# Kernel optimization log

Hardware: AMD Instinct MI355X
Metric: run time of the kernel (lower is better)

The kernel has to match this reference:

```python
import jax, jax.numpy as jnp
import numpy as np

HEADS = 16
PHI = (1.0 + np.sqrt(5.0)) / 2.0


def setup_inputs() -> dict:
    key = jax.random.key(0)
    k1, k2, k3, k4 = jax.random.split(key, 4)
    B, L, D = 2, 2048, 1024
    x = jax.random.normal(k1, (B, L, D), dtype=jnp.float32)
    # nn.Linear(dim, 3*dim, bias=False): store as [D, 3D] for x @ W
    w_qkv = jax.random.normal(k2, (D, 3 * D), dtype=jnp.float32) * (D ** -0.5)
    w_proj = jax.random.normal(k3, (D, D), dtype=jnp.float32) * (D ** -0.5)
    b_proj = jax.random.normal(k4, (D,), dtype=jnp.float32) * 0.01
    return {"x": x, "w_qkv": w_qkv, "w_proj": w_proj, "b_proj": b_proj}


def phi_bias(L):
    # pos[i] = (i * phi) mod 1 ; bias = log(exp(-|pos_i - pos_j|) + 1e-8)
    pos = (jnp.arange(L, dtype=jnp.float32) * PHI) % 1.0
    dist = jnp.abs(pos[:, None] - pos[None, :])  # [L, L]
    return jnp.log(jnp.exp(-dist) + 1e-8)


def reference(x, w_qkv, w_proj, b_proj):
    B, L, D = x.shape
    H = HEADS
    Dh = D // H
    scale = Dh ** -0.5
    qkv = (x @ w_qkv).reshape(B, L, 3, H, Dh)
    q = jnp.transpose(qkv[:, :, 0], (0, 2, 1, 3))  # [B, H, L, Dh]
    k = jnp.transpose(qkv[:, :, 1], (0, 2, 1, 3))
    v = jnp.transpose(qkv[:, :, 2], (0, 2, 1, 3))
    attn = jnp.einsum("bhid,bhjd->bhij", q, k) * scale  # [B, H, L, L]
    attn = attn + phi_bias(L)[None, None]  # additive phi-distance bias
    attn = jax.nn.softmax(attn, axis=-1)
    out = jnp.einsum("bhij,bhjd->bhid", attn, v)  # [B, H, L, Dh]
    out = jnp.transpose(out, (0, 2, 1, 3)).reshape(B, L, D)
    return out @ w_proj + b_proj
```

## Files before the change

### kernel.cpp

```cpp
#include <hip/hip_runtime.h>
#include <math.h>


typedef _Float16 f16;
typedef _Float16 f16x4 __attribute__((ext_vector_type(4)));
typedef _Float16 f16x8 __attribute__((ext_vector_type(8)));
typedef float f32x4 __attribute__((ext_vector_type(4)));

#define MFMA32(a, b, c) __builtin_amdgcn_mfma_f32_16x16x32_f16(a, b, c, 0, 0, 0)

static constexpr int Bsz = 2, Lseq = 2048, Dm = 1024, H = 16, Dh = 64;
static constexpr int Mtot = Bsz * Lseq;
static constexpr int NQKV = 3 * Dm;
static constexpr float PHI_F = 1.61803398874989484820f;
static constexpr float LOG2E = 1.44269504088896f;
static constexpr float QS = 0.125f * LOG2E;
static constexpr float CSTEP = 0.55417527999932633f;

__device__ __forceinline__ void load16_to_lds(const f16* g, f16* l) {
  __builtin_amdgcn_global_load_lds(
      (const __attribute__((address_space(1))) unsigned int*)g,
      (__attribute__((address_space(3))) unsigned int*)l, 16, 0, 0);
}

__device__ __forceinline__ void barrier_fenced() {
  __builtin_amdgcn_sched_barrier(0);
  __builtin_amdgcn_s_barrier();
  __builtin_amdgcn_sched_barrier(0);
}

__global__ __launch_bounds__(256) void prep_fused(
    const float* __restrict__ x, f16* __restrict__ xb,
    const float* __restrict__ wqkv, f16* __restrict__ wqkvT,
    const float* __restrict__ wproj, f16* __restrict__ wpT) {
  __shared__ float tile[32][33];
  int blk = blockIdx.x;
  if (blk < 4096) {
    int i = (blk * 256 + threadIdx.x) * 4;
    float4 v = *reinterpret_cast<const float4*>(x + i);
    f16 t[4] = {(f16)v.x, (f16)v.y, (f16)v.z, (f16)v.w};
    *reinterpret_cast<uint2*>(xb + i) = *reinterpret_cast<uint2*>(t);
    return;
  }
  const float* in;
  f16* out;
  int N, bx, by;
  if (blk < 7168) {
    int local = blk - 4096;
    bx = local % 96; by = local / 96; N = NQKV;
    in = wqkv; out = wqkvT;
  } else {
    int local = blk - 7168;
    bx = local & 31; by = local >> 5; N = Dm;
    in = wproj; out = wpT;
  }
  int n0 = bx * 32, k0 = by * 32;
  int tx = threadIdx.x & 31, ty = threadIdx.x >> 5;
#pragma unroll
  for (int r = 0; r < 32; r += 8)
    tile[ty + r][tx] = in[(size_t)(k0 + ty + r) * N + n0 + tx];
  __syncthreads();
#pragma unroll
  for (int r = 0; r < 32; r += 8)
    out[(size_t)(n0 + ty + r) * Dm + k0 + tx] = (f16)tile[tx][ty + r];
}

__global__ __launch_bounds__(512, 2) void gemm_qkv(
    const f16* __restrict__ A, const f16* __restrict__ Bt,
    f16* __restrict__ qb, f16* __restrict__ kb, f16* __restrict__ vb) {
  __shared__ f16 As[2 * 256 * 64];
  __shared__ f16 Bs[2 * 256 * 64];

  int tid = threadIdx.x;
  int wave = tid >> 6, lane = tid & 63;
  int quad = lane >> 4, l16 = lane & 15;
  int warp_m = wave >> 2, warp_n = wave & 3;
  int wm = warp_m * 128, wn = warp_n * 64;

  int lid = blockIdx.x;
  int xcd = lid & 7, t = lid >> 3;
  int mg = xcd >> 1, ng = xcd & 1;
  int m0 = (mg * 4 + t / 6) * 256;
  int n0 = (ng * 6 + t % 6) * 256;

  const int gu = (lane & 7) ^ (lane >> 3);
  const f16* gAb = A + (size_t)(m0 + wave * 8 + (lane >> 3)) * Dm + gu * 8;
  const f16* gBb = Bt + (size_t)(n0 + wave * 8 + (lane >> 3)) * Dm + gu * 8;

  auto stageA = [&](int buf, int h, int kn) __attribute__((always_inline)) {
#pragma unroll
    for (int i = 0; i < 2; i++)
      load16_to_lds(gAb + (size_t)(h * 128 + i * 64) * Dm + kn,
                    As + buf * 16384 + (h * 128 + i * 64 + wave * 8) * 64);
  };
  auto stageB = [&](int buf, int h, int kn) __attribute__((always_inline)) {
#pragma unroll
    for (int i = 0; i < 2; i++)
      load16_to_lds(gBb + (size_t)(h * 128 + i * 64) * Dm + kn,
                    Bs + buf * 16384 + (h * 128 + i * 64 + wave * 8) * 64);
  };

  f32x4 acc[8][4] = {};

  auto do_tile = [&](int buf, int t_) __attribute__((always_inline)) {
    const f16* Ab = As + buf * 16384 + (wm + l16) * 64;
    const f16* Bb = Bs + buf * 16384 + (wn + l16) * 64;
    int nbuf = buf ^ 1;
    int kA = ((t_ + 1) & 15) * 64;
    int kB = ((t_ + 2) & 15) * 64;

    f16x8 a[4][2], b0[2][2], b1[2][2];

#pragma unroll
    for (int m = 0; m < 4; m++)
#pragma unroll
      for (int s = 0; s < 2; s++)
        a[m][s] = *reinterpret_cast<const f16x8*>(
            Ab + m * 16 * 64 + (((s * 4 + quad) ^ (l16 & 7)) * 8));
#pragma unroll
    for (int n = 0; n < 2; n++)
#pragma unroll
      for (int s = 0; s < 2; s++)
        b0[n][s] = *reinterpret_cast<const f16x8*>(
            Bb + n * 16 * 64 + (((s * 4 + quad) ^ (l16 & 7)) * 8));
    stageA(nbuf, 0, kA);
    barrier_fenced();
    asm volatile("s_waitcnt lgkmcnt(0)" ::: "memory");
    __builtin_amdgcn_sched_barrier(0);
    __builtin_amdgcn_s_setprio(1);
#pragma unroll
    for (int m = 0; m < 4; m++)
#pragma unroll
      for (int n = 0; n < 2; n++) {
        acc[m][n] = MFMA32(a[m][0], b0[n][0], acc[m][n]);
        acc[m][n] = MFMA32(a[m][1], b0[n][1], acc[m][n]);
      }
    __builtin_amdgcn_s_setprio(0);
    barrier_fenced();

#pragma unroll
    for (int n = 0; n < 2; n++)
#pragma unroll
      for (int s = 0; s < 2; s++)
        b1[n][s] = *reinterpret_cast<const f16x8*>(
            Bb + (2 + n) * 16 * 64 + (((s * 4 + quad) ^ (l16 & 7)) * 8));
    stageA(nbuf, 1, kA);
    barrier_fenced();
    asm volatile("s_waitcnt lgkmcnt(0)" ::: "memory");
    __builtin_amdgcn_sched_barrier(0);
    __builtin_amdgcn_s_setprio(1);
#pragma unroll
    for (int m = 0; m < 4; m++)
#pragma unroll
      for (int n = 0; n < 2; n++) {
        acc[m][2 + n] = MFMA32(a[m][0], b1[n][0], acc[m][2 + n]);
        acc[m][2 + n] = MFMA32(a[m][1], b1[n][1], acc[m][2 + n]);
      }
    __builtin_amdgcn_s_setprio(0);
    barrier_fenced();

#pragma unroll
    for (int m = 0; m < 4; m++)
#pragma unroll
      for (int s = 0; s < 2; s++)
        a[m][s] = *reinterpret_cast<const f16x8*>(
            Ab + (4 + m) * 16 * 64 + (((s * 4 + quad) ^ (l16 & 7)) * 8));
    stageB(buf, 0, kB);
    barrier_fenced();
    asm volatile("s_waitcnt lgkmcnt(0)" ::: "memory");
    __builtin_amdgcn_sched_barrier(0);
    __builtin_amdgcn_s_setprio(1);
#pragma unroll
    for (int m = 0; m < 4; m++)
#pragma unroll
      for (int n = 0; n < 2; n++) {
        acc[4 + m][n] = MFMA32(a[m][0], b0[n][0], acc[4 + m][n]);
        acc[4 + m][n] = MFMA32(a[m][1], b0[n][1], acc[4 + m][n]);
      }
    __builtin_amdgcn_s_setprio(0);
    barrier_fenced();

    stageB(buf, 1, kB);
    asm volatile("s_waitcnt vmcnt(4)" ::: "memory");
    barrier_fenced();
    __builtin_amdgcn_s_setprio(1);
#pragma unroll
    for (int m = 0; m < 4; m++)
#pragma unroll
      for (int n = 0; n < 2; n++) {
        acc[4 + m][2 + n] = MFMA32(a[m][0], b1[n][0], acc[4 + m][2 + n]);
        acc[4 + m][2 + n] = MFMA32(a[m][1], b1[n][1], acc[4 + m][2 + n]);
      }
    __builtin_amdgcn_s_setprio(0);
    barrier_fenced();
  };

  stageA(0, 0, 0);
  stageA(0, 1, 0);
  stageB(0, 0, 0);
  stageB(0, 1, 0);
  stageB(1, 0, 64);
  stageB(1, 1, 64);
  asm volatile("s_waitcnt vmcnt(4)" ::: "memory");
  barrier_fenced();

#pragma unroll 1
  for (int tt = 0; tt < 16; tt += 2) {
    do_tile(0, tt);
    do_tile(1, tt + 1);
  }
  asm volatile("s_waitcnt vmcnt(0)" ::: "memory");

#pragma unroll
  for (int i = 0; i < 8; i++) {
#pragma unroll
    for (int j = 0; j < 4; j++) {
      int n = n0 + wn + j * 16 + l16;
      int ty = n >> 10;
      int df = n & 1023;
      int h = df >> 6, dh = df & 63;
      int mb = m0 + wm + i * 16 + quad * 4;
      int b = mb >> 11, l = mb & 2047;
      int bhh = b * H + h;
      if (ty == 2) {
        int jj = l & 63;
        int jh = jj >> 5, rem = jj & 31;
        int qd = (rem & 15) >> 2;
        int e0 = (rem >= 16) ? 4 : 0;
        f16x4 tmp;
#pragma unroll
        for (int r = 0; r < 4; r++) tmp[r] = (f16)acc[i][j][r];
        *reinterpret_cast<uint2*>(
            vb + (size_t)bhh * (Dh * Lseq) + (l >> 6) * 4096 + dh * 64 +
            (jh * 4 + qd) * 8 + e0) = *reinterpret_cast<uint2*>(&tmp);
      } else {
        size_t idx = (((size_t)bhh) * Lseq + l) * Dh + dh;
        if (ty == 0) {
#pragma unroll
          for (int r = 0; r < 4; r++)
            qb[idx + (size_t)r * Dh] = (f16)(acc[i][j][r] * QS);
        } else {
#pragma unroll
          for (int r = 0; r < 4; r++)
            kb[idx + (size_t)r * Dh] = (f16)acc[i][j][r];
        }
      }
    }
  }
}

__global__ __launch_bounds__(256) void gemm_proj(
    const f16* __restrict__ A, const f16* __restrict__ Bt,
    float* __restrict__ out, const float* __restrict__ bias) {
  constexpr int BM = 64, MI = 2, AI = 2;
  __shared__ f16 As[BM * 64];
  __shared__ f16 Bs[128 * 64];

  int tid = threadIdx.x;
  int wave = tid >> 6, lane = tid & 63;
  int quad = lane >> 4, l16 = lane & 15;
  int wm = (wave >> 1) * (MI * 16), wn = (wave & 1) * 64;

  int lid = blockIdx.x;
  int xcd = lid & 7, t = lid >> 3;
  int m0 = (xcd * 8 + (t >> 3)) * 64;
  int n0 = (t & 7) * 128;

  const int gu = (lane & 7) ^ (lane >> 3);
  const f16* gA[AI];
  f16* lA[AI];
#pragma unroll
  for (int i = 0; i < AI; i++) {
    int it = wave * AI + i;
    gA[i] = A + (size_t)(m0 + it * 8 + (lane >> 3)) * Dm + gu * 8;
    lA[i] = As + it * 512;
  }
  const f16* gB[4];
  f16* lB[4];
#pragma unroll
  for (int i = 0; i < 4; i++) {
    int it = wave * 4 + i;
    gB[i] = Bt + (size_t)(n0 + it * 8 + (lane >> 3)) * Dm + gu * 8;
    lB[i] = Bs + it * 512;
  }

  f32x4 acc[MI][4] = {};

  for (int k0 = 0; k0 < Dm; k0 += 64) {
#pragma unroll
    for (int i = 0; i < AI; i++) load16_to_lds(gA[i] + k0, lA[i]);
#pragma unroll
    for (int i = 0; i < 4; i++) load16_to_lds(gB[i] + k0, lB[i]);
    __syncthreads();
#pragma unroll
    for (int s = 0; s < 2; s++) {
      f16x8 a[MI], b[4];
#pragma unroll
      for (int i = 0; i < MI; i++) {
        int row = wm + i * 16 + l16;
        a[i] = *reinterpret_cast<const f16x8*>(
            As + row * 64 + (((s * 4 + quad) ^ (l16 & 7)) * 8));
      }
#pragma unroll
      for (int j = 0; j < 4; j++) {
        int row = wn + j * 16 + l16;
        b[j] = *reinterpret_cast<const f16x8*>(
            Bs + row * 64 + (((s * 4 + quad) ^ (l16 & 7)) * 8));
      }
#pragma unroll
      for (int i = 0; i < MI; i++)
#pragma unroll
        for (int j = 0; j < 4; j++)
          acc[i][j] = MFMA32(a[i], b[j], acc[i][j]);
    }
    __syncthreads();
  }

#pragma unroll
  for (int i = 0; i < MI; i++)
#pragma unroll
    for (int j = 0; j < 4; j++) {
      int n = n0 + wn + j * 16 + l16;
#pragma unroll
      for (int r = 0; r < 4; r++) {
        int m = m0 + wm + i * 16 + quad * 4 + r;
        out[(size_t)m * Dm + n] = acc[i][j][r] + bias[n];
      }
    }
}

__global__ __launch_bounds__(512, 4) void attn_kernel(
    const f16* __restrict__ qb,
    const f16* __restrict__ kb,
    const f16* __restrict__ vb,
    f16* __restrict__ ctx) {
  __shared__ __align__(16) unsigned char smem[33280];
  f16* Ks = (f16*)smem;
  f16* Vs = (f16*)(smem + 8192);

  int id = blockIdx.x;
  int bh = (id & 7) * 4 + ((id >> 3) >> 4);
  int q0 = ((id >> 3) & 15) * 128;

  int tid = threadIdx.x, wave = tid >> 6, lane = tid & 63;
  int quad = lane >> 4, l16 = lane & 15;
  int jhalf = wave >> 2, qq = wave & 3;

  f16x8 qfrag[2][2];
  float pq[2];
#pragma unroll
  for (int set = 0; set < 2; set++) {
    int q = q0 + qq * 32 + set * 16 + l16;
    const f16* Qrow = qb + ((size_t)bh * Lseq + q) * Dh;
    qfrag[set][0] = *reinterpret_cast<const f16x8*>(Qrow + quad * 8);
    qfrag[set][1] = *reinterpret_cast<const f16x8*>(Qrow + 32 + quad * 8);
    pq[set] = fmodf((float)q * PHI_F, 1.0f);
  }

  float pk[2][4];
#pragma unroll
  for (int jb = 0; jb < 2; jb++)
#pragma unroll
    for (int r = 0; r < 4; r++) {
      int j = jhalf * 32 + jb * 16 + quad * 4 + r;
      pk[jb][r] = fmodf((float)j * PHI_F, 1.0f);
    }

  const f16* Kbh = kb + (size_t)bh * Lseq * Dh;
  const f16* Vbh = vb + (size_t)bh * Dh * Lseq;
  const int gu = (lane & 7) ^ (lane >> 3);
  int g8 = wave * 8 + (lane >> 3);
  const f16* gK = Kbh + (size_t)g8 * Dh + gu * 8;
  const f16* gV = Vbh + (size_t)g8 * 64 + gu * 8;
  f16* lK = Ks + wave * 512;
  f16* lV = Vs + wave * 512;

  const f16 one = (f16)1.0f;
  const f16x8 ones8 = {one, one, one, one, one, one, one, one};

  f32x4 acc_o[2][4] = {};
  f32x4 acc_l[2] = {};

  for (int j0 = 0; j0 < Lseq; j0 += 64) {
    __syncthreads();
    load16_to_lds(gK + (size_t)j0 * Dh, lK);
    load16_to_lds(gV + (size_t)j0 * 64, lV);
    __syncthreads();

    f32x4 accs[2][2] = {};
#pragma unroll
    for (int s = 0; s < 2; s++)
#pragma unroll
      for (int jb = 0; jb < 2; jb++) {
        f16x8 kf = *reinterpret_cast<const f16x8*>(
            Ks + (jhalf * 32 + jb * 16 + l16) * 64 + (((s * 4 + quad) ^ (l16 & 7)) * 8));
        accs[0][jb] = MFMA32(kf, qfrag[0][s], accs[0][jb]);
        accs[1][jb] = MFMA32(kf, qfrag[1][s], accs[1][jb]);
      }

    f16x8 pf8[2];
#pragma unroll
    for (int set = 0; set < 2; set++) {
#pragma unroll
      for (int jb = 0; jb < 2; jb++) {
        float p[4];
#pragma unroll
        for (int r = 0; r < 4; r++) {
          float d = pq[set] - pk[jb][r];
          float arg = fmaf(-LOG2E, fabsf(d), accs[set][jb][r]);
          p[r] = __builtin_amdgcn_exp2f(arg);
        }
        auto lo = __builtin_amdgcn_cvt_pkrtz(p[0], p[1]);
        auto hi = __builtin_amdgcn_cvt_pkrtz(p[2], p[3]);
        pf8[set][jb * 4 + 0] = lo[0];
        pf8[set][jb * 4 + 1] = lo[1];
        pf8[set][jb * 4 + 2] = hi[0];
        pf8[set][jb * 4 + 3] = hi[1];
      }
      acc_l[set] = MFMA32(ones8, pf8[set], acc_l[set]);
    }
#pragma unroll
    for (int jb = 0; jb < 2; jb++)
#pragma unroll
      for (int r = 0; r < 4; r++)
        pk[jb][r] = __builtin_amdgcn_fractf(pk[jb][r] + CSTEP);

#pragma unroll
    for (int dblk = 0; dblk < 4; dblk++) {
      int row = dblk * 16 + l16;
      f16x8 va = *reinterpret_cast<const f16x8*>(
          Vs + row * 64 + (((jhalf * 4 + quad) ^ (l16 & 7)) * 8));
      acc_o[0][dblk] = MFMA32(va, pf8[0], acc_o[0][dblk]);
      acc_o[1][dblk] = MFMA32(va, pf8[1], acc_o[1][dblk]);
    }
  }

  __syncthreads();
  float* Oex = (float*)smem;
  float* Lex = (float*)(smem + 32768);
  if (jhalf == 1) {
#pragma unroll
    for (int set = 0; set < 2; set++) {
#pragma unroll
      for (int dblk = 0; dblk < 4; dblk++)
#pragma unroll
        for (int r = 0; r < 4; r++)
          Oex[(((qq * 2 + set) * 4 + dblk) * 16 + quad * 4 + r) * 16 + l16] =
              acc_o[set][dblk][r];
      if (quad == 0) Lex[(qq * 2 + set) * 16 + l16] = acc_l[set][0];
    }
  }
  __syncthreads();
  if (jhalf == 0) {
    int b = bh >> 4, h = bh & 15;
#pragma unroll
    for (int set = 0; set < 2; set++) {
      float ltot = acc_l[set][0] + Lex[(qq * 2 + set) * 16 + l16];
      float inv = 1.0f / ltot;
      int q = q0 + qq * 32 + set * 16 + l16;
      f16* crow = ctx + (size_t)(b * Lseq + q) * Dm + h * 64;
#pragma unroll
      for (int dblk = 0; dblk < 4; dblk++) {
        f16x4 o;
#pragma unroll
        for (int r = 0; r < 4; r++) {
          float full = acc_o[set][dblk][r] +
              Oex[(((qq * 2 + set) * 4 + dblk) * 16 + quad * 4 + r) * 16 + l16];
          o[r] = (f16)(full * inv);
        }
        *reinterpret_cast<uint2*>(crow + dblk * 16 + quad * 4) =
            *reinterpret_cast<uint2*>(&o);
      }
    }
  }
}

extern "C" void kernel_launch(void* const* d_in, const int* in_sizes, int n_in,
                              void* d_out, int out_size, void* d_ws, size_t ws_size,
                              hipStream_t stream) {
  const float* x      = (const float*)d_in[0];
  const float* w_qkv  = (const float*)d_in[1];
  const float* w_proj = (const float*)d_in[2];
  const float* b_proj = (const float*)d_in[3];
  float* out = (float*)d_out;

  f16* xb    = (f16*)d_ws;
  f16* wqkvT = xb + (size_t)Mtot * Dm;
  f16* wpT   = wqkvT + (size_t)NQKV * Dm;
  f16* qb    = wpT + (size_t)Dm * Dm;
  f16* kb    = qb + (size_t)Bsz * H * Lseq * Dh;
  f16* vb    = kb + (size_t)Bsz * H * Lseq * Dh;
  f16* ctx   = vb + (size_t)Bsz * H * Lseq * Dh;

  prep_fused<<<8192, 256, 0, stream>>>(x, xb, w_qkv, wqkvT, w_proj, wpT);

  gemm_qkv<<<192, 512, 0, stream>>>(xb, wqkvT, qb, kb, vb);

  attn_kernel<<<512, 512, 0, stream>>>(qb, kb, vb, ctx);

  gemm_proj<<<512, 256, 0, stream>>>(ctx, wpT, out, b_proj);
}
```

Baseline: 179.9 us.

## Retile QKV GEMM to 256x192 blocks so 256 blocks fill all CUs

Shrinks the QKV projection GEMM block tile from 256x256 to 256x192, so the grid grows from 192 to 256 blocks and maps onto all 256 compute units. The B staging, the MFMA loops, the accumulator shape, the vmcnt waits and the XCD-aware block swizzle are all reworked to match. This removes idle CUs in a single-wave launch, at the cost of lower arithmetic intensity per block and launch bounds relaxed to one block per CU.

```diff
diff --git a/kernel.cpp b/kernel.cpp
--- a/kernel.cpp
+++ b/kernel.cpp
@@ -65,23 +65,23 @@
     out[(size_t)(n0 + ty + r) * Dm + k0 + tx] = (f16)tile[tx][ty + r];
 }
 
-__global__ __launch_bounds__(512, 2) void gemm_qkv(
+__global__ __launch_bounds__(512, 1) void gemm_qkv(
     const f16* __restrict__ A, const f16* __restrict__ Bt,
     f16* __restrict__ qb, f16* __restrict__ kb, f16* __restrict__ vb) {
   __shared__ f16 As[2 * 256 * 64];
-  __shared__ f16 Bs[2 * 256 * 64];
+  __shared__ f16 Bs[2 * 192 * 64];
 
   int tid = threadIdx.x;
   int wave = tid >> 6, lane = tid & 63;
   int quad = lane >> 4, l16 = lane & 15;
   int warp_m = wave >> 2, warp_n = wave & 3;
-  int wm = warp_m * 128, wn = warp_n * 64;
+  int wm = warp_m * 128, wn = warp_n * 48;
 
   int lid = blockIdx.x;
   int xcd = lid & 7, t = lid >> 3;
-  int mg = xcd >> 1, ng = xcd & 1;
-  int m0 = (mg * 4 + t / 6) * 256;
-  int n0 = (ng * 6 + t % 6) * 256;
+  int mg = xcd & 3, ng = xcd >> 2;
+  int m0 = (mg * 4 + (t >> 3)) * 256;
+  int n0 = (ng * 8 + (t & 7)) * 192;
 
   const int gu = (lane & 7) ^ (lane >> 3);
   const f16* gAb = A + (size_t)(m0 + wave * 8 + (lane >> 3)) * Dm + gu * 8;
@@ -93,23 +93,28 @@
       load16_to_lds(gAb + (size_t)(h * 128 + i * 64) * Dm + kn,
                     As + buf * 16384 + (h * 128 + i * 64 + wave * 8) * 64);
   };
-  auto stageB = [&](int buf, int h, int kn) __attribute__((always_inline)) {
-#pragma unroll
-    for (int i = 0; i < 2; i++)
-      load16_to_lds(gBb + (size_t)(h * 128 + i * 64) * Dm + kn,
-                    Bs + buf * 16384 + (h * 128 + i * 64 + wave * 8) * 64);
+  auto stageB = [&](int buf, int part, int kn) __attribute__((always_inline)) {
+    if (part == 0) {
+#pragma unroll
+      for (int i = 0; i < 2; i++)
+        load16_to_lds(gBb + (size_t)(i * 64) * Dm + kn,
+                      Bs + buf * 12288 + (i * 64 + wave * 8) * 64);
+    } else {
+      load16_to_lds(gBb + (size_t)128 * Dm + kn,
+                    Bs + buf * 12288 + (128 + wave * 8) * 64);
+    }
   };
 
-  f32x4 acc[8][4] = {};
+  f32x4 acc[8][3] = {};
 
   auto do_tile = [&](int buf, int t_) __attribute__((always_inline)) {
     const f16* Ab = As + buf * 16384 + (wm + l16) * 64;
-    const f16* Bb = Bs + buf * 16384 + (wn + l16) * 64;
+    const f16* Bb = Bs + buf * 12288 + (wn + l16) * 64;
     int nbuf = buf ^ 1;
     int kA = ((t_ + 1) & 15) * 64;
     int kB = ((t_ + 2) & 15) * 64;
 
-    f16x8 a[4][2], b0[2][2], b1[2][2];
+    f16x8 a[4][2], b0[2][2], b1[2];
 
 #pragma unroll
     for (int m = 0; m < 4; m++)
@@ -139,23 +144,19 @@
     barrier_fenced();
 
 #pragma unroll
-    for (int n = 0; n < 2; n++)
-#pragma unroll
-      for (int s = 0; s < 2; s++)
-        b1[n][s] = *reinterpret_cast<const f16x8*>(
-            Bb + (2 + n) * 16 * 64 + (((s * 4 + quad) ^ (l16 & 7)) * 8));
+    for (int s = 0; s < 2; s++)
+      b1[s] = *reinterpret_cast<const f16x8*>(
+          Bb + 2 * 16 * 64 + (((s * 4 + quad) ^ (l16 & 7)) * 8));
     stageA(nbuf, 1, kA);
     barrier_fenced();
     asm volatile("s_waitcnt lgkmcnt(0)" ::: "memory");
     __builtin_amdgcn_sched_barrier(0);
     __builtin_amdgcn_s_setprio(1);
 #pragma unroll
-    for (int m = 0; m < 4; m++)
-#pragma unroll
-      for (int n = 0; n < 2; n++) {
-        acc[m][2 + n] = MFMA32(a[m][0], b1[n][0], acc[m][2 + n]);
-        acc[m][2 + n] = MFMA32(a[m][1], b1[n][1], acc[m][2 + n]);
-      }
+    for (int m = 0; m < 4; m++) {
+      acc[m][2] = MFMA32(a[m][0], b1[0], acc[m][2]);
+      acc[m][2] = MFMA32(a[m][1], b1[1], acc[m][2]);
+    }
     __builtin_amdgcn_s_setprio(0);
     barrier_fenced();
 
@@ -181,16 +182,14 @@
     barrier_fenced();
 
     stageB(buf, 1, kB);
-    asm volatile("s_waitcnt vmcnt(4)" ::: "memory");
+    asm volatile("s_waitcnt vmcnt(3)" ::: "memory");
     barrier_fenced();
     __builtin_amdgcn_s_setprio(1);
 #pragma unroll
-    for (int m = 0; m < 4; m++)
-#pragma unroll
-      for (int n = 0; n < 2; n++) {
-        acc[4 + m][2 + n] = MFMA32(a[m][0], b1[n][0], acc[4 + m][2 + n]);
-        acc[4 + m][2 + n] = MFMA32(a[m][1], b1[n][1], acc[4 + m][2 + n]);
-      }
+    for (int m = 0; m < 4; m++) {
+      acc[4 + m][2] = MFMA32(a[m][0], b1[0], acc[4 + m][2]);
+      acc[4 + m][2] = MFMA32(a[m][1], b1[1], acc[4 + m][2]);
+    }
     __builtin_amdgcn_s_setprio(0);
     barrier_fenced();
   };
@@ -201,7 +200,7 @@
   stageB(0, 1, 0);
   stageB(1, 0, 64);
   stageB(1, 1, 64);
-  asm volatile("s_waitcnt vmcnt(4)" ::: "memory");
+  asm volatile("s_waitcnt vmcnt(3)" ::: "memory");
   barrier_fenced();
 
 #pragma unroll 1
@@ -214,7 +213,7 @@
 #pragma unroll
   for (int i = 0; i < 8; i++) {
 #pragma unroll
-    for (int j = 0; j < 4; j++) {
+    for (int j = 0; j < 3; j++) {
       int n = n0 + wn + j * 16 + l16;
       int ty = n >> 10;
       int df = n & 1023;
@@ -494,7 +493,7 @@
 
   prep_fused<<<8192, 256, 0, stream>>>(x, xb, w_qkv, wqkvT, w_proj, wpT);
 
-  gemm_qkv<<<192, 512, 0, stream>>>(xb, wqkvT, qb, kb, vb);
+  gemm_qkv<<<256, 512, 0, stream>>>(xb, wqkvT, qb, kb, vb);
 
   attn_kernel<<<512, 512, 0, stream>>>(qb, kb, vb, ctx);
 
```

Result: no change. 177.0 us (-1.6%).
